# Kernel optimization log

Hardware: AMD Instinct MI355X
Metric: run time of the kernel (lower is better)

## Reference

```python
import jax, jax.numpy as jnp
import numpy as np


def setup_inputs() -> dict:
    key = jax.random.key(0)
    ks = jax.random.split(key, 5)
    B, M, R = 32, 32, 128
    d_lang, d_region, d_rank, d_fusion = 1024, 2048, 256, 256
    u = jax.random.normal(ks[0], (B, M, d_lang), dtype=jnp.float32)
    v = jax.random.normal(ks[1], (B, R, d_region), dtype=jnp.float32)
    # Linear weights stored torch-style as (out_features, in_features)
    Wu = jax.random.normal(ks[2], (d_rank, d_lang), dtype=jnp.float32) * (1.0 / np.sqrt(d_lang))
    Wv = jax.random.normal(ks[3], (d_rank, d_region), dtype=jnp.float32) * (1.0 / np.sqrt(d_region))
    Wp = jax.random.normal(ks[4], (d_fusion, d_rank), dtype=jnp.float32) * (1.0 / np.sqrt(d_rank))
    bp = jnp.zeros((d_fusion,), dtype=jnp.float32)
    return {"u": u, "v": v, "Wu": Wu, "Wv": Wv, "Wp": Wp, "bp": bp}


def reference(u, v, Wu, Wv, Wp, bp):
    # u: (B, M, d_lang), v: (B, R, d_region)
    up = jnp.einsum('bmd,rd->bmr', u, Wu)          # (B, M, d_rank)  [rd: out x in]
    vp = jnp.einsum('bnd,rd->bnr', v, Wv)          # (B, R, d_rank)
    # broadcast bilinear multiply: (B, M, R, d_rank)
    prod = up[:, :, None, :] * vp[:, None, :, :]
    o = jnp.einsum('bmnk,fk->bmnf', prod, Wp) + bp  # p-linear -> (B, M, R, d_fusion)
    # dropout is identity in inference mode
    return jax.nn.relu(o)
```

## Files before the change

### kernel.cpp

```cpp
#include <hip/hip_runtime.h>
#include <hip/hip_bf16.h>


typedef __attribute__((ext_vector_type(8))) short short8;
typedef __attribute__((ext_vector_type(4))) float floatx4;
typedef __attribute__((ext_vector_type(4))) unsigned uintx4;

__device__ __forceinline__ short f2bf(float f) {
    union { float f; unsigned u; } cv; cv.f = f;
    unsigned r = cv.u + 0x7fffu + ((cv.u >> 16) & 1u);
    return (short)(r >> 16);
}
__device__ __forceinline__ unsigned pack_rne(float x, float y) {
    __hip_bfloat162 h = __float22bfloat162_rn(make_float2(x, y));
    union { __hip_bfloat162 h; unsigned u; } cv; cv.h = h;
    return cv.u;
}
__device__ __forceinline__ unsigned scale2_rne(short a, short b, float ua, float ub) {
    float x = __uint_as_float(((unsigned)(unsigned short)a) << 16) * ua;
    float y = __uint_as_float(((unsigned)(unsigned short)b) << 16) * ub;
    return pack_rne(x, y);
}

#define MFMA16(a, b, c) __builtin_amdgcn_mfma_f32_16x16x32_bf16((a), (b), (c), 0, 0, 0)

__global__ __launch_bounds__(256) void proj_kernel(
    const float* __restrict__ u, const float* __restrict__ Wu,
    float* __restrict__ upf,
    const float* __restrict__ v, const float* __restrict__ Wv,
    short* __restrict__ vpb,
    const float* __restrict__ Wp, short* __restrict__ Wp_bf)
{
    __shared__ __align__(16) short Xs[2][32 * 64];
    __shared__ __align__(16) short Wsh[2][64 * 64];

    const int tid  = threadIdx.x;
    const int lane = tid & 63;
    const int wave = tid >> 6;
    const int quad = lane >> 4;
    const int l15  = lane & 15;

    const int bid = blockIdx.x;

    if (bid < 32) {
        const int widx = (bid * 256 + tid) * 8;
        float4 g0 = *(const float4*)(Wp + widx);
        float4 g1 = *(const float4*)(Wp + widx + 4);
        short8 o;
        o[0] = f2bf(g0.x); o[1] = f2bf(g0.y); o[2] = f2bf(g0.z); o[3] = f2bf(g0.w);
        o[4] = f2bf(g1.x); o[5] = f2bf(g1.y); o[6] = f2bf(g1.z); o[7] = f2bf(g1.w);
        *(short8*)(Wp_bf + widx) = o;
    }

    const int xcd = bid & 7, j = bid >> 3;
    const int cb  = j & 3;
    const int pidx = xcd + 8 * (j >> 2);
    const float *X, *W; int D, r0; bool is_u;
    if (pidx < 32) { is_u = true;  X = u; W = Wu; D = 1024; r0 = pidx * 32; }
    else           { is_u = false; X = v; W = Wv; D = 2048; r0 = (pidx - 32) * 32; }
    const int c0 = cb * 64;
    const int wr = (wave >> 1) * 16;
    const int wc = (wave & 1) * 32;

    const int xr_ = tid >> 3, xk = (tid & 7) * 8;
    const int wr_ = tid >> 2, wk = (tid & 3) * 16;
    const float* xg = X + (size_t)(r0 + xr_) * D + xk;
    const float* wg = W + (size_t)(c0 + wr_) * D + wk;
    const int xswz  = (xr_ & 7) << 4;
    const int wswz  = (wr_ & 7) << 4;
    const int xbase = xr_ * 128 + xk * 2;
    const int wbase = wr_ * 128 + wk * 2;

    floatx4 acc[2] = {};
    float4 x0, x1, y0, y1, y2, y3;

#define LDC(k)                                                                  \
    x0 = *(const float4*)(xg + (k));      x1 = *(const float4*)(xg + (k) + 4);  \
    y0 = *(const float4*)(wg + (k));      y1 = *(const float4*)(wg + (k) + 4);  \
    y2 = *(const float4*)(wg + (k) + 8);  y3 = *(const float4*)(wg + (k) + 12);

#define PKC(bi)                                                                 \
    { char* xb = (char*)&Xs[bi][0]; char* wb = (char*)&Wsh[bi][0]; uintx4 q;    \
      q[0] = pack_rne(x0.x, x0.y); q[1] = pack_rne(x0.z, x0.w);                 \
      q[2] = pack_rne(x1.x, x1.y); q[3] = pack_rne(x1.z, x1.w);                 \
      *(uintx4*)(xb + (xbase ^ xswz)) = q;                                      \
      q[0] = pack_rne(y0.x, y0.y); q[1] = pack_rne(y0.z, y0.w);                 \
      q[2] = pack_rne(y1.x, y1.y); q[3] = pack_rne(y1.z, y1.w);                 \
      *(uintx4*)(wb + (wbase ^ wswz)) = q;                                      \
      q[0] = pack_rne(y2.x, y2.y); q[1] = pack_rne(y2.z, y2.w);                 \
      q[2] = pack_rne(y3.x, y3.y); q[3] = pack_rne(y3.z, y3.w);                 \
      *(uintx4*)(wb + ((wbase + 16) ^ wswz)) = q; }

    LDC(0); PKC(0);
    __syncthreads();

    const int asw = (l15 & 7) << 4;
    int cur = 0;
    for (int kc = 0; kc < D; kc += 64) {
        const bool has = (kc + 64) < D;
        if (has) { LDC(kc + 64); }

        const char* xb = (const char*)&Xs[cur][0];
        const char* wb = (const char*)&Wsh[cur][0];
        short8 a0  = *(const short8*)(xb + (((wr + l15) * 128 +      quad * 16) ^ asw));
        short8 a1  = *(const short8*)(xb + (((wr + l15) * 128 + 64 + quad * 16) ^ asw));
        short8 b00 = *(const short8*)(wb + (((wc +      l15) * 128 +      quad * 16) ^ asw));
        short8 b01 = *(const short8*)(wb + (((wc +      l15) * 128 + 64 + quad * 16) ^ asw));
        short8 b10 = *(const short8*)(wb + (((wc + 16 + l15) * 128 +      quad * 16) ^ asw));
        short8 b11 = *(const short8*)(wb + (((wc + 16 + l15) * 128 + 64 + quad * 16) ^ asw));
        acc[0] = MFMA16(a0, b00, acc[0]);
        acc[1] = MFMA16(a0, b10, acc[1]);
        acc[0] = MFMA16(a1, b01, acc[0]);
        acc[1] = MFMA16(a1, b11, acc[1]);

        if (has) { PKC(cur ^ 1); }
        __syncthreads();
        cur ^= 1;
    }
#undef LDC
#undef PKC

    if (is_u) {
#pragma unroll
        for (int tf = 0; tf < 2; tf++)
#pragma unroll
            for (int r = 0; r < 4; r++) {
                const int row = r0 + wr + quad * 4 + r;
                const int col = c0 + wc + tf * 16 + l15;
                upf[(size_t)row * 256 + col] = acc[tf][r];
            }
    } else {
#pragma unroll
        for (int tf = 0; tf < 2; tf++)
#pragma unroll
            for (int r = 0; r < 4; r++) {
                const int row = r0 + wr + quad * 4 + r;
                const int col = c0 + wc + tf * 16 + l15;
                vpb[(size_t)row * 256 + col] = f2bf(acc[tf][r]);
            }
    }
}

__global__ __launch_bounds__(256, 4) void bilinear_kernel(
    const float* __restrict__ up, const short* __restrict__ vp,
    const short* __restrict__ Wp_bf, const float* __restrict__ bp,
    float* __restrict__ out)
{
    __shared__ __align__(16) short A_lds[64 * 256];
    __shared__ float up_s[256];

    const int tid  = threadIdx.x;
    const int lane = tid & 63;
    const int wave = tid >> 6;
    const int quad = lane >> 4;
    const int l15  = lane & 15;

    const int bid = blockIdx.x;
    const int xcd = bid & 7;
    const int grp = bid >> 3;
    const int s   = grp & 63;
    const int b   = (grp >> 6) * 8 + xcd;
    const int m   = s >> 1;
    const int nh  = s & 1;
    const int bm  = b * 32 + m;

    up_s[tid] = up[(size_t)bm * 256 + tid];

    const int kw = wave * 64;
    const short* vsrc = vp + (size_t)(b * 128 + nh * 64 + lane) * 256 + kw;
    short8 vv[8];
#pragma unroll
    for (int i = 0; i < 8; i++) vv[i] = *(const short8*)(vsrc + i * 8);

    __syncthreads();

    {
        char* Ab = (char*)A_lds;
        const int rsw   = (lane & 7) << 4;
        const int rbase = lane * 512 + kw * 2;
#pragma unroll
        for (int i = 0; i < 8; i++) {
            const float4 ua = *(const float4*)&up_s[kw + i * 8];
            const float4 ub = *(const float4*)&up_s[kw + i * 8 + 4];
            uintx4 o;
            o[0] = scale2_rne(vv[i][0], vv[i][1], ua.x, ua.y);
            o[1] = scale2_rne(vv[i][2], vv[i][3], ua.z, ua.w);
            o[2] = scale2_rne(vv[i][4], vv[i][5], ub.x, ub.y);
            o[3] = scale2_rne(vv[i][6], vv[i][7], ub.z, ub.w);
            *(uintx4*)(Ab + ((rbase + i * 16) ^ rsw)) = o;
        }
    }
    __syncthreads();

    floatx4 acc[4][4] = {};
    const char* Ab = (const char*)A_lds;
    const int aswz = (l15 & 7) << 4;
    const int wf   = wave * 64;
    const short* wq = Wp_bf + (size_t)(wf + l15) * 256 + quad * 8;

    short8 bcur[4], bnxt[4];
#pragma unroll
    for (int tt = 0; tt < 4; tt++)
        bcur[tt] = *(const short8*)(wq + tt * 4096);

#pragma unroll
    for (int kc = 0; kc < 256; kc += 32) {
        if (kc < 224) {
#pragma unroll
            for (int tt = 0; tt < 4; tt++)
                bnxt[tt] = *(const short8*)(wq + tt * 4096 + kc + 32);
        }
        short8 a[4];
#pragma unroll
        for (int tt = 0; tt < 4; tt++) {
            const int row = tt * 16 + l15;
            a[tt] = *(const short8*)(Ab + ((row * 512 + kc * 2 + quad * 16) ^ aswz));
        }
        __builtin_amdgcn_s_setprio(1);
#pragma unroll
        for (int tn = 0; tn < 4; tn++)
#pragma unroll
            for (int tf = 0; tf < 4; tf++)
                acc[tn][tf] = MFMA16(bcur[tf], a[tn], acc[tn][tf]);
        __builtin_amdgcn_s_setprio(0);
        if (kc < 224) {
#pragma unroll
            for (int tt = 0; tt < 4; tt++) bcur[tt] = bnxt[tt];
        }
    }

    float4 bpv[4];
#pragma unroll
    for (int tf = 0; tf < 4; tf++)
        bpv[tf] = *(const float4*)&bp[wf + tf * 16 + quad * 4];

    const size_t out_base = (size_t)bm * 128 * 256 + (size_t)nh * 64 * 256;
#pragma unroll
    for (int tn = 0; tn < 4; tn++) {
        const int n = tn * 16 + l15;
        float* orow = out + out_base + (size_t)n * 256 + wf + quad * 4;
#pragma unroll
        for (int tf = 0; tf < 4; tf++) {
            float4 vo;
            vo.x = fmaxf(acc[tn][tf][0] + bpv[tf].x, 0.0f);
            vo.y = fmaxf(acc[tn][tf][1] + bpv[tf].y, 0.0f);
            vo.z = fmaxf(acc[tn][tf][2] + bpv[tf].z, 0.0f);
            vo.w = fmaxf(acc[tn][tf][3] + bpv[tf].w, 0.0f);
            *(float4*)(orow + tf * 16) = vo;
        }
    }
}

extern "C" void kernel_launch(void* const* d_in, const int* in_sizes, int n_in,
                              void* d_out, int out_size, void* d_ws, size_t ws_size,
                              hipStream_t stream) {
    const float* u  = (const float*)d_in[0];
    const float* v  = (const float*)d_in[1];
    const float* Wu = (const float*)d_in[2];
    const float* Wv = (const float*)d_in[3];
    const float* Wp = (const float*)d_in[4];
    const float* bp = (const float*)d_in[5];
    float* out = (float*)d_out;

    float* up_f  = (float*)d_ws;
    short* vp_bf = (short*)(up_f + 262144);
    short* Wp_bf = vp_bf + 1048576;

    proj_kernel<<<dim3(640), dim3(256), 0, stream>>>(
        u, Wu, up_f, v, Wv, vp_bf, Wp, Wp_bf);
    bilinear_kernel<<<dim3(2048), dim3(256), 0, stream>>>(
        up_f, vp_bf, Wp_bf, bp, out);
}
```

Baseline: 230.8 us.

## Build A operand in registers from global loads, dropping LDS staging

The bilinear kernel no longer stages the scaled vp*up tile in shared memory behind two barriers. Each wave now loads its own vp fragments and up values straight from global memory every k-step, scales them in registers and feeds the MFMA directly. This removes the LDS writes, reads and syncs and may raise occupancy. In exchange, all four waves redundantly load and scale the same vp rows, global loads sit in the inner loop, and the explicit double-buffered Wp prefetch is replaced by unroll 2.

New measurement: 258.6 us. +12.0%, slower.

```diff
diff --git a/kernel.cpp b/kernel.cpp
--- a/kernel.cpp
+++ b/kernel.cpp
@@ -146,9 +146,6 @@
     const short* __restrict__ Wp_bf, const float* __restrict__ bp,
     float* __restrict__ out)
 {
-    __shared__ __align__(16) short A_lds[64 * 256];
-    __shared__ float up_s[256];
-
     const int tid  = threadIdx.x;
     const int lane = tid & 63;
     const int wave = tid >> 6;
@@ -163,70 +160,42 @@
     const int m   = s >> 1;
     const int nh  = s & 1;
     const int bm  = b * 32 + m;
-
-    up_s[tid] = up[(size_t)bm * 256 + tid];
-
-    const int kw = wave * 64;
-    const short* vsrc = vp + (size_t)(b * 128 + nh * 64 + lane) * 256 + kw;
-    short8 vv[8];
-#pragma unroll
-    for (int i = 0; i < 8; i++) vv[i] = *(const short8*)(vsrc + i * 8);
-
-    __syncthreads();
-
-    {
-        char* Ab = (char*)A_lds;
-        const int rsw   = (lane & 7) << 4;
-        const int rbase = lane * 512 + kw * 2;
-#pragma unroll
-        for (int i = 0; i < 8; i++) {
-            const float4 ua = *(const float4*)&up_s[kw + i * 8];
-            const float4 ub = *(const float4*)&up_s[kw + i * 8 + 4];
+    const int n0  = nh * 64;
+    const int wf  = wave * 64;
+
+    const short* vrow = vp + (size_t)(b * 128 + n0 + l15) * 256 + quad * 8;
+    const float* urow = up + (size_t)bm * 256 + quad * 8;
+    const short* wrow = Wp_bf + (size_t)(wf + l15) * 256 + quad * 8;
+
+    floatx4 acc[4][4] = {};
+
+#pragma unroll 2
+    for (int kc = 0; kc < 256; kc += 32) {
+        const float4 u0 = *(const float4*)(urow + kc);
+        const float4 u1 = *(const float4*)(urow + kc + 4);
+        short8 bb[4];
+#pragma unroll
+        for (int tt = 0; tt < 4; tt++)
+            bb[tt] = *(const short8*)(wrow + tt * 4096 + kc);
+        short8 a[4];
+#pragma unroll
+        for (int tt = 0; tt < 4; tt++) {
+            short8 vv = *(const short8*)(vrow + tt * 4096 + kc);
             uintx4 o;
-            o[0] = scale2_rne(vv[i][0], vv[i][1], ua.x, ua.y);
-            o[1] = scale2_rne(vv[i][2], vv[i][3], ua.z, ua.w);
-            o[2] = scale2_rne(vv[i][4], vv[i][5], ub.x, ub.y);
-            o[3] = scale2_rne(vv[i][6], vv[i][7], ub.z, ub.w);
-            *(uintx4*)(Ab + ((rbase + i * 16) ^ rsw)) = o;
-        }
-    }
-    __syncthreads();
-
-    floatx4 acc[4][4] = {};
-    const char* Ab = (const char*)A_lds;
-    const int aswz = (l15 & 7) << 4;
-    const int wf   = wave * 64;
-    const short* wq = Wp_bf + (size_t)(wf + l15) * 256 + quad * 8;
-
-    short8 bcur[4], bnxt[4];
-#pragma unroll
-    for (int tt = 0; tt < 4; tt++)
-        bcur[tt] = *(const short8*)(wq + tt * 4096);
-
-#pragma unroll
-    for (int kc = 0; kc < 256; kc += 32) {
-        if (kc < 224) {
-#pragma unroll
-            for (int tt = 0; tt < 4; tt++)
-                bnxt[tt] = *(const short8*)(wq + tt * 4096 + kc + 32);
-        }
-        short8 a[4];
-#pragma unroll
-        for (int tt = 0; tt < 4; tt++) {
-            const int row = tt * 16 + l15;
-            a[tt] = *(const short8*)(Ab + ((row * 512 + kc * 2 + quad * 16) ^ aswz));
+            o[0] = scale2_rne(vv[0], vv[1], u0.x, u0.y);
+            o[1] = scale2_rne(vv[2], vv[3], u0.z, u0.w);
+            o[2] = scale2_rne(vv[4], vv[5], u1.x, u1.y);
+            o[3] = scale2_rne(vv[6], vv[7], u1.z, u1.w);
+            union { uintx4 u; short8 s; } cv; cv.u = o;
+            a[tt] = cv.s;
         }
         __builtin_amdgcn_s_setprio(1);
 #pragma unroll
         for (int tn = 0; tn < 4; tn++)
 #pragma unroll
             for (int tf = 0; tf < 4; tf++)
-                acc[tn][tf] = MFMA16(bcur[tf], a[tn], acc[tn][tf]);
+                acc[tn][tf] = MFMA16(bb[tf], a[tn], acc[tn][tf]);
         __builtin_amdgcn_s_setprio(0);
-        if (kc < 224) {
-#pragma unroll
-            for (int tt = 0; tt < 4; tt++) bcur[tt] = bnxt[tt];
-        }
     }
 
     float4 bpv[4];
@@ -234,7 +203,7 @@
     for (int tf = 0; tf < 4; tf++)
         bpv[tf] = *(const float4*)&bp[wf + tf * 16 + quad * 4];
 
-    const size_t out_base = (size_t)bm * 128 * 256 + (size_t)nh * 64 * 256;
+    const size_t out_base = (size_t)bm * 128 * 256 + (size_t)n0 * 256;
 #pragma unroll
     for (int tn = 0; tn < 4; tn++) {
         const int n = tn * 16 + l15;
```

## Pre-convert inputs to bf16 and stage projection GEMM tiles via global_load_lds

Applied to the files above, without the earlier changes.

Adds a separate pass that converts u, v, Wu, Wv and Wp to bf16 in the workspace. The projection kernel then loads bf16 tiles straight into LDS with global_load_lds, using an XOR-swizzled layout and a larger 64x128 tile per block with 2x4 MFMAs per wave, instead of converting fp32 in registers. This removes the per-element packing from the GEMM loop and raises data reuse. In exchange it adds an extra launch and a full read/write pass over v (~32MB fp32 read plus 16MB written), and the projection grid shrinks to 160 blocks, which lowers parallelism.

Result: slower. 235.5 us (+2.0%).

```diff
diff --git a/kernel.cpp b/kernel.cpp
--- a/kernel.cpp
+++ b/kernel.cpp
@@ -22,17 +22,52 @@
     return pack_rne(x, y);
 }
 
+#define GL2LDS(gptr, lptr) __builtin_amdgcn_global_load_lds(                    \
+    (const __attribute__((address_space(1))) void*)(gptr),                      \
+    (__attribute__((address_space(3))) void*)(lptr), 16, 0, 0)
+
 #define MFMA16(a, b, c) __builtin_amdgcn_mfma_f32_16x16x32_bf16((a), (b), (c), 0, 0, 0)
 
+#define N_U  1048576
+#define N_V  8388608
+#define N_WU 262144
+#define N_WV 524288
+#define N_WP 65536
+
+__global__ __launch_bounds__(256) void convert_kernel(
+    const float* __restrict__ u, const float* __restrict__ v,
+    const float* __restrict__ Wu, const float* __restrict__ Wv,
+    const float* __restrict__ Wp, short* __restrict__ dst)
+{
+    const int n_u = N_U / 4, n_v = N_V / 4, n_wu = N_WU / 4, n_wv = N_WV / 4,
+              n_wp = N_WP / 4;
+    const int total = n_u + n_v + n_wu + n_wv + n_wp;
+    for (int i4 = blockIdx.x * blockDim.x + threadIdx.x; i4 < total;
+         i4 += gridDim.x * blockDim.x) {
+        const float* src; int off = i4;
+        if (off < n_u) src = u;
+        else { off -= n_u;
+            if (off < n_v) src = v;
+            else { off -= n_v;
+                if (off < n_wu) src = Wu;
+                else { off -= n_wu;
+                    if (off < n_wv) src = Wv;
+                    else { off -= n_wv; src = Wp; } } } }
+        float4 f = *((const float4*)src + off);
+        short4 o;
+        o.x = f2bf(f.x); o.y = f2bf(f.y); o.z = f2bf(f.z); o.w = f2bf(f.w);
+        *((short4*)dst + i4) = o;
+    }
+}
+
 __global__ __launch_bounds__(256) void proj_kernel(
-    const float* __restrict__ u, const float* __restrict__ Wu,
+    const short* __restrict__ Xu, const short* __restrict__ Wgu,
     float* __restrict__ upf,
-    const float* __restrict__ v, const float* __restrict__ Wv,
-    short* __restrict__ vpb,
-    const float* __restrict__ Wp, short* __restrict__ Wp_bf)
+    const short* __restrict__ Xv, const short* __restrict__ Wgv,
+    short* __restrict__ vpb)
 {
-    __shared__ __align__(16) short Xs[2][32 * 64];
-    __shared__ __align__(16) short Wsh[2][64 * 64];
+    __shared__ __align__(16) short Xs[2][64 * 32];
+    __shared__ __align__(16) short Wsh[2][128 * 32];
 
     const int tid  = threadIdx.x;
     const int lane = tid & 63;
@@ -41,103 +76,86 @@
     const int l15  = lane & 15;
 
     const int bid = blockIdx.x;
-
-    if (bid < 32) {
-        const int widx = (bid * 256 + tid) * 8;
-        float4 g0 = *(const float4*)(Wp + widx);
-        float4 g1 = *(const float4*)(Wp + widx + 4);
-        short8 o;
-        o[0] = f2bf(g0.x); o[1] = f2bf(g0.y); o[2] = f2bf(g0.z); o[3] = f2bf(g0.w);
-        o[4] = f2bf(g1.x); o[5] = f2bf(g1.y); o[6] = f2bf(g1.z); o[7] = f2bf(g1.w);
-        *(short8*)(Wp_bf + widx) = o;
-    }
-
-    const int xcd = bid & 7, j = bid >> 3;
-    const int cb  = j & 3;
-    const int pidx = xcd + 8 * (j >> 2);
-    const float *X, *W; int D, r0; bool is_u;
-    if (pidx < 32) { is_u = true;  X = u; W = Wu; D = 1024; r0 = pidx * 32; }
-    else           { is_u = false; X = v; W = Wv; D = 2048; r0 = (pidx - 32) * 32; }
-    const int c0 = cb * 64;
-    const int wr = (wave >> 1) * 16;
-    const int wc = (wave & 1) * 32;
-
-    const int xr_ = tid >> 3, xk = (tid & 7) * 8;
-    const int wr_ = tid >> 2, wk = (tid & 3) * 16;
-    const float* xg = X + (size_t)(r0 + xr_) * D + xk;
-    const float* wg = W + (size_t)(c0 + wr_) * D + wk;
-    const int xswz  = (xr_ & 7) << 4;
-    const int wswz  = (wr_ & 7) << 4;
-    const int xbase = xr_ * 128 + xk * 2;
-    const int wbase = wr_ * 128 + wk * 2;
-
-    floatx4 acc[2] = {};
-    float4 x0, x1, y0, y1, y2, y3;
-
-#define LDC(k)                                                                  \
-    x0 = *(const float4*)(xg + (k));      x1 = *(const float4*)(xg + (k) + 4);  \
-    y0 = *(const float4*)(wg + (k));      y1 = *(const float4*)(wg + (k) + 4);  \
-    y2 = *(const float4*)(wg + (k) + 8);  y3 = *(const float4*)(wg + (k) + 12);
-
-#define PKC(bi)                                                                 \
-    { char* xb = (char*)&Xs[bi][0]; char* wb = (char*)&Wsh[bi][0]; uintx4 q;    \
-      q[0] = pack_rne(x0.x, x0.y); q[1] = pack_rne(x0.z, x0.w);                 \
-      q[2] = pack_rne(x1.x, x1.y); q[3] = pack_rne(x1.z, x1.w);                 \
-      *(uintx4*)(xb + (xbase ^ xswz)) = q;                                      \
-      q[0] = pack_rne(y0.x, y0.y); q[1] = pack_rne(y0.z, y0.w);                 \
-      q[2] = pack_rne(y1.x, y1.y); q[3] = pack_rne(y1.z, y1.w);                 \
-      *(uintx4*)(wb + (wbase ^ wswz)) = q;                                      \
-      q[0] = pack_rne(y2.x, y2.y); q[1] = pack_rne(y2.z, y2.w);                 \
-      q[2] = pack_rne(y3.x, y3.y); q[3] = pack_rne(y3.z, y3.w);                 \
-      *(uintx4*)(wb + ((wbase + 16) ^ wswz)) = q; }
-
-    LDC(0); PKC(0);
+    const short *X, *W; int D; bool is_u; int xcd, t;
+    if (bid < 128) {
+        is_u = false; X = Xv; W = Wgv; D = 2048;
+        xcd = bid & 7; t = bid >> 3;
+    } else {
+        is_u = true;  X = Xu; W = Wgu; D = 1024;
+        const int lb = bid - 128;
+        xcd = lb & 7; t = lb >> 3;
+    }
+    const int cp = t & 1;
+    const int rp = (t >> 1) * 8 + xcd;
+    const int r0 = rp * 64;
+    const int c0 = cp * 128;
+    const int wm  = (wave >> 1) * 32;
+    const int wn2 = (wave & 1) * 64;
+
+    const int srow = tid >> 2, sq = tid & 3;
+    const int qg = sq ^ ((srow >> 1) & 3);
+    const short* xg  = X + (size_t)(r0 + srow) * D + qg * 8;
+    const short* wg0 = W + (size_t)(c0 + srow) * D + qg * 8;
+    const short* wg1 = W + (size_t)(c0 + 64 + srow) * D + qg * 8;
+    const int sxo = tid * 8;
+
+#define PSTG(bi, kc)                                                            \
+    { GL2LDS(xg  + (kc), &Xs[bi][sxo]);                                         \
+      GL2LDS(wg0 + (kc), &Wsh[bi][sxo]);                                        \
+      GL2LDS(wg1 + (kc), &Wsh[bi][2048 + sxo]); }
+
+    floatx4 acc[2][4] = {};
+    const int aslot = (quad ^ ((l15 >> 1) & 3)) * 8;
+
+    PSTG(0, 0);
     __syncthreads();
 
-    const int asw = (l15 & 7) << 4;
     int cur = 0;
-    for (int kc = 0; kc < D; kc += 64) {
-        const bool has = (kc + 64) < D;
-        if (has) { LDC(kc + 64); }
-
-        const char* xb = (const char*)&Xs[cur][0];
-        const char* wb = (const char*)&Wsh[cur][0];
-        short8 a0  = *(const short8*)(xb + (((wr + l15) * 128 +      quad * 16) ^ asw));
-        short8 a1  = *(const short8*)(xb + (((wr + l15) * 128 + 64 + quad * 16) ^ asw));
-        short8 b00 = *(const short8*)(wb + (((wc +      l15) * 128 +      quad * 16) ^ asw));
-        short8 b01 = *(const short8*)(wb + (((wc +      l15) * 128 + 64 + quad * 16) ^ asw));
-        short8 b10 = *(const short8*)(wb + (((wc + 16 + l15) * 128 +      quad * 16) ^ asw));
-        short8 b11 = *(const short8*)(wb + (((wc + 16 + l15) * 128 + 64 + quad * 16) ^ asw));
-        acc[0] = MFMA16(a0, b00, acc[0]);
-        acc[1] = MFMA16(a0, b10, acc[1]);
-        acc[0] = MFMA16(a1, b01, acc[0]);
-        acc[1] = MFMA16(a1, b11, acc[1]);
-
-        if (has) { PKC(cur ^ 1); }
+    for (int kc = 0; kc < D; kc += 32) {
+        if (kc + 32 < D) { PSTG(cur ^ 1, kc + 32); }
+
+        const short* xb = &Xs[cur][0];
+        const short* wb = &Wsh[cur][0];
+        short8 a[2], bfr[4];
+#pragma unroll
+        for (int tm = 0; tm < 2; tm++)
+            a[tm] = *(const short8*)&xb[(wm + tm * 16 + l15) * 32 + aslot];
+#pragma unroll
+        for (int tn = 0; tn < 4; tn++)
+            bfr[tn] = *(const short8*)&wb[(wn2 + tn * 16 + l15) * 32 + aslot];
+#pragma unroll
+        for (int tm = 0; tm < 2; tm++)
+#pragma unroll
+            for (int tn = 0; tn < 4; tn++)
+                acc[tm][tn] = MFMA16(a[tm], bfr[tn], acc[tm][tn]);
+
         __syncthreads();
         cur ^= 1;
     }
-#undef LDC
-#undef PKC
+#undef PSTG
 
     if (is_u) {
 #pragma unroll
-        for (int tf = 0; tf < 2; tf++)
-#pragma unroll
-            for (int r = 0; r < 4; r++) {
-                const int row = r0 + wr + quad * 4 + r;
-                const int col = c0 + wc + tf * 16 + l15;
-                upf[(size_t)row * 256 + col] = acc[tf][r];
-            }
+        for (int tm = 0; tm < 2; tm++)
+#pragma unroll
+            for (int tn = 0; tn < 4; tn++)
+#pragma unroll
+                for (int r = 0; r < 4; r++) {
+                    const int row = r0 + wm + tm * 16 + quad * 4 + r;
+                    const int col = c0 + wn2 + tn * 16 + l15;
+                    upf[(size_t)row * 256 + col] = acc[tm][tn][r];
+                }
     } else {
 #pragma unroll
-        for (int tf = 0; tf < 2; tf++)
-#pragma unroll
-            for (int r = 0; r < 4; r++) {
-                const int row = r0 + wr + quad * 4 + r;
-                const int col = c0 + wc + tf * 16 + l15;
-                vpb[(size_t)row * 256 + col] = f2bf(acc[tf][r]);
-            }
+        for (int tm = 0; tm < 2; tm++)
+#pragma unroll
+            for (int tn = 0; tn < 4; tn++)
+#pragma unroll
+                for (int r = 0; r < 4; r++) {
+                    const int row = r0 + wm + tm * 16 + quad * 4 + r;
+                    const int col = c0 + wn2 + tn * 16 + l15;
+                    vpb[(size_t)row * 256 + col] = f2bf(acc[tm][tn][r]);
+                }
     }
 }
 
@@ -234,7 +252,7 @@
     for (int tf = 0; tf < 4; tf++)
         bpv[tf] = *(const float4*)&bp[wf + tf * 16 + quad * 4];
 
-    const size_t out_base = (size_t)bm * 128 * 256 + (size_t)nh * 64 * 256;
+    const size_t out_base = (size_t)bm * 128 * 256 + (size_t)(nh * 64) * 256;
 #pragma unroll
     for (int tn = 0; tn < 4; tn++) {
         const int n = tn * 16 + l15;
@@ -262,12 +280,18 @@
     const float* bp = (const float*)d_in[5];
     float* out = (float*)d_out;
 
-    float* up_f  = (float*)d_ws;
+    short* bf    = (short*)d_ws;
+    short* u_bf  = bf;
+    short* v_bf  = u_bf + N_U;
+    short* Wu_bf = v_bf + N_V;
+    short* Wv_bf = Wu_bf + N_WU;
+    short* Wp_bf = Wv_bf + N_WV;
+    float* up_f  = (float*)(Wp_bf + N_WP);
     short* vp_bf = (short*)(up_f + 262144);
-    short* Wp_bf = vp_bf + 1048576;
-
-    proj_kernel<<<dim3(640), dim3(256), 0, stream>>>(
-        u, Wu, up_f, v, Wv, vp_bf, Wp, Wp_bf);
+
+    convert_kernel<<<dim3(2048), dim3(256), 0, stream>>>(u, v, Wu, Wv, Wp, bf);
+    proj_kernel<<<dim3(160), dim3(256), 0, stream>>>(
+        u_bf, Wu_bf, up_f, v_bf, Wv_bf, vp_bf);
     bilinear_kernel<<<dim3(2048), dim3(256), 0, stream>>>(
         up_f, vp_bf, Wp_bf, bp, out);
 }
```
